# Kernel optimization log

Measured on AMD Instinct MI355X. Metric: run time of the kernel, lower is better.

Reference implementation:

```python
import jax, jax.numpy as jnp
from jax import lax
import numpy as np

TAPS = 4          # db2 filter length
LEVEL = 4
CH = 32
SLOPE = 10.0      # sigmoid sharpness of learned hard-threshold activation

# db2 decomposition low-pass coefficients (pywt convention)
_DB2 = np.array([-0.12940952255126037, 0.2241438680420134,
                 0.8365163037378079, 0.48296291314453416], dtype=np.float32)

def setup_inputs() -> dict:
    key = jax.random.key(0)
    k1, k2, k3 = jax.random.split(key, 3)
    x = jax.random.normal(k1, (128, CH, 4096), dtype=jnp.float32)
    # learned per-channel, per-level low-pass kernels: db2 init + small perturbation
    h_lo = jnp.asarray(_DB2)[None, None, :] + 0.02 * jax.random.normal(
        k2, (CH, LEVEL, TAPS), dtype=jnp.float32)
    # learned symmetric thresholds (Act_Init=0 -> small positive values)
    bias = 0.1 * jax.random.uniform(k3, (CH, LEVEL), dtype=jnp.float32)
    return {"x": x, "h_lo": h_lo, "bias": bias}

def _grouped_dwt_step(a, k_lo, k_hi):
    # a: [B,C,T]; kernels: [C,1,taps]; circular boundary, stride-2 downsample
    B, C, T = a.shape
    a_pad = jnp.concatenate([a, a[..., : TAPS - 1]], axis=-1)  # circular pad
    dn = ('NCH', 'OIH', 'NCH')
    lo = lax.conv_general_dilated(a_pad, k_lo, (2,), 'VALID',
                                  dimension_numbers=dn, feature_group_count=C)
    hi = lax.conv_general_dilated(a_pad, k_hi, (2,), 'VALID',
                                  dimension_numbers=dn, feature_group_count=C)
    return lo, hi  # each [B,C,T//2]

def reference(x, h_lo, bias):
    """Batched learned wavelet decomposition (all channels at once via grouped conv).
    Returns coefficients packed along last dim: [yl, d_L, ..., d_1] -> [B,C,T].
    """
    B, C, T = x.shape
    sign = ((-1.0) ** jnp.arange(TAPS)).astype(x.dtype)  # QMF sign flip
    a = x
    details = []
    for l in range(LEVEL):
        k_lo = h_lo[:, l, :][:, None, :]                       # [C,1,taps]
        k_hi = (sign * h_lo[:, l, ::-1])[:, None, :]           # high-pass via QMF
        a, hi = _grouped_dwt_step(a, k_lo, k_hi)
        b = bias[None, :, l, None]                             # [1,C,1]
        # symmetric sigmoid (soft hard-threshold) activation on detail coeffs
        d = hi * (jax.nn.sigmoid(SLOPE * (hi - b)) + jax.nn.sigmoid(-SLOPE * (hi + b)))
        details.append(d)
    # pack: approximation (coarsest) first, then details coarsest->finest
    return jnp.concatenate([a] + details[::-1], axis=-1)
```

## Files before the change

### kernel.cpp

```cpp
#include <hip/hip_runtime.h>
#include <math.h>

#define BATCH 128
#define CHANS 32
#define TLEN 4096
#define LEVELS 4
#define NTAPS 4
#define SLOPE 10.0f

__global__ __launch_bounds__(256) void lwpt_kernel(
    const float* __restrict__ x, const float* __restrict__ h_lo,
    const float* __restrict__ bias, float* __restrict__ out)
{
    __shared__ float buf0[TLEN];
    __shared__ float buf1[TLEN / 2];

    const int bc  = blockIdx.x;
    const int c   = bc & (CHANS - 1);
    const int tid = threadIdx.x;

    const float4* xin = (const float4*)(x + (size_t)bc * TLEN);
    float4* b0v = (float4*)buf0;
    #pragma unroll
    for (int k = 0; k < TLEN / 4 / 256; ++k)
        b0v[tid + k * 256] = xin[tid + k * 256];
    __syncthreads();

    float* src = buf0;
    float* dst = buf1;
    float* orow = out + (size_t)bc * TLEN;

    #pragma unroll
    for (int l = 0; l < LEVELS; ++l) {
        const int Tl = TLEN >> l;
        const int To = Tl >> 1;

        const float k0 = h_lo[(c * LEVELS + l) * NTAPS + 0];
        const float k1 = h_lo[(c * LEVELS + l) * NTAPS + 1];
        const float k2 = h_lo[(c * LEVELS + l) * NTAPS + 2];
        const float k3 = h_lo[(c * LEVELS + l) * NTAPS + 3];
        const float bl = bias[c * LEVELS + l];

        for (int t = tid; t < To; t += 256) {
            const int i0 = 2 * t;
            const float a0 = src[i0];
            const float a1 = src[i0 + 1];
            const float a2 = src[(i0 + 2 >= Tl) ? (i0 + 2 - Tl) : (i0 + 2)];
            const float a3 = src[(i0 + 3 >= Tl) ? (i0 + 3 - Tl) : (i0 + 3)];

            const float lo = a0 * k0 + a1 * k1 + a2 * k2 + a3 * k3;
            const float hi = a0 * k3 - a1 * k2 + a2 * k1 - a3 * k0;

            dst[t] = lo;

            const float s1 = 1.0f / (1.0f + __expf(-SLOPE * (hi - bl)));
            const float s2 = 1.0f / (1.0f + __expf( SLOPE * (hi + bl)));
            orow[To + t] = hi * (s1 + s2);
        }
        __syncthreads();
        float* tmp = src; src = dst; dst = tmp;
    }

    if (tid < (TLEN >> LEVELS))
        orow[tid] = src[tid];
}

extern "C" void kernel_launch(void* const* d_in, const int* in_sizes, int n_in,
                              void* d_out, int out_size, void* d_ws, size_t ws_size,
                              hipStream_t stream) {
    const float* x    = (const float*)d_in[0];
    const float* h_lo = (const float*)d_in[1];
    const float* bias = (const float*)d_in[2];
    float* out = (float*)d_out;

    dim3 grid(BATCH * CHANS);
    dim3 block(256);
    lwpt_kernel<<<grid, block, 0, stream>>>(x, h_lo, bias, out);
}
```

Measured before the change: 31.15 us.

## Register-block DWT levels, compute level 0 from global, fuse sigmoid gates

Rewrites the kernel so each thread computes a fixed contiguous chunk of outputs per level with all levels fully unrolled. Level 0 now reads the input straight from global memory into registers with float4 loads, so the shared-memory staging copy of the whole row is gone and shared memory drops to 12KB. Detail stores are vectorised. The two sigmoids are merged into one expression that needs a single reciprocal, with clamping to keep exp in range. In exchange, global reads are per-thread strided chunks rather than fully lane-contiguous, and the extra halo reads duplicate some traffic.

```diff
diff --git a/kernel.cpp b/kernel.cpp
--- a/kernel.cpp
+++ b/kernel.cpp
@@ -1,68 +1,122 @@
 #include <hip/hip_runtime.h>
 #include <math.h>
 
-#define BATCH 128
-#define CHANS 32
 #define TLEN 4096
 #define LEVELS 4
-#define NTAPS 4
+#define CHANS 32
 #define SLOPE 10.0f
+
+__device__ __forceinline__ float sgate(float hi, float b) {
+    const float za = fminf(fmaxf(-SLOPE * (hi - b), -30.f), 30.f);
+    const float zb = fminf(fmaxf( SLOPE * (hi + b), -30.f), 30.f);
+    const float ea = __expf(za);
+    const float eb = __expf(zb);
+    return hi * (2.f + ea + eb) * __builtin_amdgcn_rcpf((1.f + ea) * (1.f + eb));
+}
 
 __global__ __launch_bounds__(256) void lwpt_kernel(
     const float* __restrict__ x, const float* __restrict__ h_lo,
     const float* __restrict__ bias, float* __restrict__ out)
 {
-    __shared__ float buf0[TLEN];
-    __shared__ float buf1[TLEN / 2];
+    __shared__ float bufA[2048];
+    __shared__ float bufB[1024];
 
     const int bc  = blockIdx.x;
     const int c   = bc & (CHANS - 1);
     const int tid = threadIdx.x;
 
-    const float4* xin = (const float4*)(x + (size_t)bc * TLEN);
-    float4* b0v = (float4*)buf0;
-    #pragma unroll
-    for (int k = 0; k < TLEN / 4 / 256; ++k)
-        b0v[tid + k * 256] = xin[tid + k * 256];
+    const float* xrow = x   + (size_t)bc * TLEN;
+    float*       orow = out + (size_t)bc * TLEN;
+
+    const float4 k0v = ((const float4*)h_lo)[c * LEVELS + 0];
+    const float4 k1v = ((const float4*)h_lo)[c * LEVELS + 1];
+    const float4 k2v = ((const float4*)h_lo)[c * LEVELS + 2];
+    const float4 k3v = ((const float4*)h_lo)[c * LEVELS + 3];
+    const float b0 = bias[c * LEVELS + 0];
+    const float b1 = bias[c * LEVELS + 1];
+    const float b2 = bias[c * LEVELS + 2];
+    const float b3 = bias[c * LEVELS + 3];
+
+    {
+        const float4* x4 = (const float4*)xrow;
+        float in[18];
+        #pragma unroll
+        for (int k = 0; k < 4; ++k) {
+            const float4 v = x4[4 * tid + k];
+            in[4*k+0] = v.x; in[4*k+1] = v.y; in[4*k+2] = v.z; in[4*k+3] = v.w;
+        }
+        const float2 e = *(const float2*)(xrow + ((16 * tid + 16) & (TLEN - 1)));
+        in[16] = e.x; in[17] = e.y;
+
+        float lo[8], dd[8];
+        #pragma unroll
+        for (int j = 0; j < 8; ++j) {
+            const float a0 = in[2*j], a1 = in[2*j+1], a2 = in[2*j+2], a3 = in[2*j+3];
+            lo[j] = a0*k0v.x + a1*k0v.y + a2*k0v.z + a3*k0v.w;
+            const float hi = a0*k0v.w - a1*k0v.z + a2*k0v.y - a3*k0v.x;
+            dd[j] = sgate(hi, b0);
+        }
+        ((float4*)bufA)[2*tid]   = make_float4(lo[0], lo[1], lo[2], lo[3]);
+        ((float4*)bufA)[2*tid+1] = make_float4(lo[4], lo[5], lo[6], lo[7]);
+        float4* o4 = (float4*)(orow + 2048);
+        o4[2*tid]   = make_float4(dd[0], dd[1], dd[2], dd[3]);
+        o4[2*tid+1] = make_float4(dd[4], dd[5], dd[6], dd[7]);
+    }
     __syncthreads();
 
-    float* src = buf0;
-    float* dst = buf1;
-    float* orow = out + (size_t)bc * TLEN;
+    {
+        float in[10];
+        #pragma unroll
+        for (int k = 0; k < 2; ++k) {
+            const float4 v = ((const float4*)bufA)[2 * tid + k];
+            in[4*k+0] = v.x; in[4*k+1] = v.y; in[4*k+2] = v.z; in[4*k+3] = v.w;
+        }
+        const float2 e = *(const float2*)(bufA + ((8 * tid + 8) & 2047));
+        in[8] = e.x; in[9] = e.y;
 
-    #pragma unroll
-    for (int l = 0; l < LEVELS; ++l) {
-        const int Tl = TLEN >> l;
-        const int To = Tl >> 1;
+        float lo[4], dd[4];
+        #pragma unroll
+        for (int j = 0; j < 4; ++j) {
+            const float a0 = in[2*j], a1 = in[2*j+1], a2 = in[2*j+2], a3 = in[2*j+3];
+            lo[j] = a0*k1v.x + a1*k1v.y + a2*k1v.z + a3*k1v.w;
+            const float hi = a0*k1v.w - a1*k1v.z + a2*k1v.y - a3*k1v.x;
+            dd[j] = sgate(hi, b1);
+        }
+        ((float4*)bufB)[tid] = make_float4(lo[0], lo[1], lo[2], lo[3]);
+        ((float4*)(orow + 1024))[tid] = make_float4(dd[0], dd[1], dd[2], dd[3]);
+    }
+    __syncthreads();
 
-        const float k0 = h_lo[(c * LEVELS + l) * NTAPS + 0];
-        const float k1 = h_lo[(c * LEVELS + l) * NTAPS + 1];
-        const float k2 = h_lo[(c * LEVELS + l) * NTAPS + 2];
-        const float k3 = h_lo[(c * LEVELS + l) * NTAPS + 3];
-        const float bl = bias[c * LEVELS + l];
+    {
+        float in[6];
+        const float4 v = ((const float4*)bufB)[tid];
+        in[0] = v.x; in[1] = v.y; in[2] = v.z; in[3] = v.w;
+        const float2 e = *(const float2*)(bufB + ((4 * tid + 4) & 1023));
+        in[4] = e.x; in[5] = e.y;
 
-        for (int t = tid; t < To; t += 256) {
-            const int i0 = 2 * t;
-            const float a0 = src[i0];
-            const float a1 = src[i0 + 1];
-            const float a2 = src[(i0 + 2 >= Tl) ? (i0 + 2 - Tl) : (i0 + 2)];
-            const float a3 = src[(i0 + 3 >= Tl) ? (i0 + 3 - Tl) : (i0 + 3)];
+        float lo[2], dd[2];
+        #pragma unroll
+        for (int j = 0; j < 2; ++j) {
+            const float a0 = in[2*j], a1 = in[2*j+1], a2 = in[2*j+2], a3 = in[2*j+3];
+            lo[j] = a0*k2v.x + a1*k2v.y + a2*k2v.z + a3*k2v.w;
+            const float hi = a0*k2v.w - a1*k2v.z + a2*k2v.y - a3*k2v.x;
+            dd[j] = sgate(hi, b2);
+        }
+        ((float2*)bufA)[tid] = make_float2(lo[0], lo[1]);
+        ((float2*)(orow + 512))[tid] = make_float2(dd[0], dd[1]);
+    }
+    __syncthreads();
 
-            const float lo = a0 * k0 + a1 * k1 + a2 * k2 + a3 * k3;
-            const float hi = a0 * k3 - a1 * k2 + a2 * k1 - a3 * k0;
-
-            dst[t] = lo;
-
-            const float s1 = 1.0f / (1.0f + __expf(-SLOPE * (hi - bl)));
-            const float s2 = 1.0f / (1.0f + __expf( SLOPE * (hi + bl)));
-            orow[To + t] = hi * (s1 + s2);
-        }
-        __syncthreads();
-        float* tmp = src; src = dst; dst = tmp;
+    {
+        const float a0 = bufA[2 * tid];
+        const float a1 = bufA[2 * tid + 1];
+        const float2 e = *(const float2*)(bufA + ((2 * tid + 2) & 511));
+        const float a2 = e.x, a3 = e.y;
+        const float lo = a0*k3v.x + a1*k3v.y + a2*k3v.z + a3*k3v.w;
+        const float hi = a0*k3v.w - a1*k3v.z + a2*k3v.y - a3*k3v.x;
+        orow[tid]       = lo;
+        orow[256 + tid] = sgate(hi, b3);
     }
-
-    if (tid < (TLEN >> LEVELS))
-        orow[tid] = src[tid];
 }
 
 extern "C" void kernel_launch(void* const* d_in, const int* in_sizes, int n_in,
@@ -73,7 +127,7 @@
     const float* bias = (const float*)d_in[2];
     float* out = (float*)d_out;
 
-    dim3 grid(BATCH * CHANS);
+    dim3 grid(128 * CHANS);
     dim3 block(256);
     lwpt_kernel<<<grid, block, 0, stream>>>(x, h_lo, bias, out);
 }
```

New measurement: 26.08 us. 1.19x faster.
